# Kernel optimization log

Measured on AMD Instinct MI355X. Metric: run time of the kernel, lower is better.

## Reference

```python
import jax, jax.numpy as jnp
import numpy as np

N_HEAD = 12


def setup_inputs() -> dict:
    key = jax.random.key(0)
    ks = jax.random.split(key, 16)
    B, N, D, P, H = 1, 512, 384, 128, N_HEAD
    s = 0.02
    return {
        'x1d': jax.random.normal(ks[0], (B, N, D), jnp.float32),
        'x2d': jax.random.normal(ks[1], (B, N, N, P), jnp.float32),
        'pose_t': jax.random.normal(ks[2], (B, N, 3), jnp.float32),
        'pose_r': jax.random.normal(ks[3], (B, N, 3, 3), jnp.float32),
        'bias': jnp.zeros((B, 1, N, N), jnp.float32),
        'w_sq': jax.random.normal(ks[4], (D, D), jnp.float32) * s,
        'w_sk': jax.random.normal(ks[5], (D, D), jnp.float32) * s,
        'w_sv': jax.random.normal(ks[6], (D, D), jnp.float32) * s,
        'w_pb': jax.random.normal(ks[7], (P, H), jnp.float32) * s,
        'w_pq': jax.random.normal(ks[8], (D, H * 3 * 4), jnp.float32) * s,
        'w_pk': jax.random.normal(ks[9], (D, H * 3 * 4), jnp.float32) * s,
        'w_pv': jax.random.normal(ks[10], (D, H * 3 * 8), jnp.float32) * s,
        'tpw': jax.random.uniform(ks[11], (H,), jnp.float32),
        'w_pairv': jax.random.normal(ks[12], (P, D), jnp.float32) * s,
        'w_out': jax.random.normal(ks[13], (2 * D + H * 8 * 4, D), jnp.float32) * s,
        'b_out': jnp.zeros((D,), jnp.float32),
    }


def reference(x1d, x2d, pose_t, pose_r, bias, w_sq, w_sk, w_sv, w_pb,
              w_pq, w_pk, w_pv, tpw, w_pairv, w_out, b_out):
    B, N, D = x1d.shape
    H = N_HEAD
    dk = D // H
    scalar_w = 1.0 / np.sqrt(3 * dk)
    point_w_c = 1.0 / np.sqrt(3 * 4 * 9 / 2)
    pair_w = 1.0 / np.sqrt(3)

    T = pose_t                                # [B,N,3]
    R = jnp.swapaxes(pose_r, -1, -2)          # [B,N,3,3] (pose[1]^T as in torch code)

    # scalar attention
    q_s = (x1d @ w_sq).reshape(B, N, H, dk)
    k_s = (x1d @ w_sk).reshape(B, N, H, dk)
    v_s = (x1d @ w_sv).reshape(B, N, H, dk)
    scalar_attn = jnp.einsum('bihc,bjhc->bhij', q_s * scalar_w, k_s)

    # point attention (global frame)
    def affine(pt):  # R @ pt + T
        return jnp.einsum('bnxy,bnhpy->bnhpx', R, pt) + T[:, :, None, None, :]

    q_p = affine((x1d @ w_pq).reshape(B, N, H, 4, 3))
    k_p = affine((x1d @ w_pk).reshape(B, N, H, 4, 3))
    v_p = affine((x1d @ w_pv).reshape(B, N, H, 8, 3))

    dist = jnp.linalg.norm(q_p[:, :, None] - k_p[:, None], axis=-1)  # [B,I,J,H,P]
    pw = point_w_c * jax.nn.softplus(tpw)                            # [H]
    point_attn = -0.5 * pw[:, None, None] * jnp.transpose(dist.sum(-1), (0, 3, 1, 2))

    # pair bias attention
    pair_attn = pair_w * jnp.transpose(x2d @ w_pb, (0, 3, 1, 2))     # [B,H,I,J]

    attn = jax.nn.softmax(scalar_attn + point_attn + pair_attn + bias, axis=-1)

    # aggregations
    out_scalar = jnp.einsum('bhij,bjhc->bihc', attn, v_s).reshape(B, N, D)

    out_pg = jnp.einsum('bhij,bjhcp->bihcp', attn, v_p)              # [B,I,H,8,3]
    # inverse affine: R^T @ (x - T)
    out_pl = jnp.einsum('bnyx,bnhpy->bnhpx', R, out_pg - T[:, :, None, None, :])
    out_pn = jnp.linalg.norm(out_pl, axis=-1).reshape(B, N, H * 8)
    out_pl = out_pl.reshape(B, N, H * 8 * 3)

    v_pair = (x2d @ w_pairv).reshape(B, N, N, H, dk)
    out_pair = jnp.einsum('bhij,bijhc->bihc', attn, v_pair).reshape(B, N, D)

    feat = jnp.concatenate([out_scalar, out_pl, out_pair, out_pn], axis=-1)
    return feat @ w_out + b_out
```

## Files before the change

### kernel.cpp

```cpp
#include <hip/hip_runtime.h>
#include <hip/hip_bf16.h>
#include <math.h>

#define N_  512
#define D_  384
#define H_  12
#define DK_ 32
#define P_  128

typedef short short8 __attribute__((ext_vector_type(8)));
typedef float f32x4  __attribute__((ext_vector_type(4)));

static __device__ __forceinline__ unsigned short f2bf(float f) {
    union { float f; unsigned int u; } v; v.f = f;
    unsigned int r = (v.u + 0x7FFFu + ((v.u >> 16) & 1u)) >> 16;
    return (unsigned short)r;
}
static __device__ __forceinline__ float bf2f(unsigned short u) {
    union { unsigned int u; float f; } v; v.u = ((unsigned int)u) << 16;
    return v.f;
}
static __device__ __forceinline__ short2 pk2bf(float a, float b) {
    __hip_bfloat162 h = __float22bfloat162_rn(make_float2(a, b));
    return *(short2*)&h;
}
typedef union { short8 v; short2 h2[4]; } s8u;

__global__ __launch_bounds__(384) void k_front(
    const float* __restrict__ x2d, const float* __restrict__ w_pb,
    float* __restrict__ pairlog,
    const float* __restrict__ x1d, const float* __restrict__ pose_t,
    const float* __restrict__ pose_r,
    const float* __restrict__ w_sq, const float* __restrict__ w_sk,
    const float* __restrict__ w_sv, const float* __restrict__ w_pq,
    const float* __restrict__ w_pk, const float* __restrict__ w_pv,
    float* __restrict__ qs, float* __restrict__ kst,
    float* __restrict__ qp, float* __restrict__ kpt,
    unsigned short* __restrict__ vcatT)
{
    __shared__ float raw[8][288];
    __shared__ float Rsh[8][9];
    __shared__ float Tsh[8][3];

    const int t = threadIdx.x;

    if (blockIdx.x < 2048) {
        if (t >= 256) return;
        const int wid  = t >> 6;
        const int lane = t & 63;
        const int quad = lane >> 4;
        const int col  = lane & 15;
        const float pair_w = 0.57735027f;

        short8 bfr[4];
        #pragma unroll
        for (int kt = 0; kt < 4; ++kt) {
            #pragma unroll
            for (int jj = 0; jj < 8; ++jj) {
                int p = kt * 32 + quad * 8 + jj;
                bfr[kt][jj] = (col < 12) ? (short)f2bf(w_pb[p * 12 + col]) : (short)0;
            }
        }
        #pragma unroll
        for (int s = 0; s < 2; ++s) {
            const int T  = blockIdx.x * 8 + wid * 2 + s;
            const int i  = T >> 5;
            const int j0 = (T & 31) << 4;
            const float* xrow = x2d + ((size_t)(i * N_) + j0 + col) * P_;

            f32x4 acc = {0.f, 0.f, 0.f, 0.f};
            #pragma unroll
            for (int kt = 0; kt < 4; ++kt) {
                const int k0 = kt * 32 + quad * 8;
                float4 f0 = *(const float4*)(xrow + k0);
                float4 f1 = *(const float4*)(xrow + k0 + 4);
                s8u afr;
                afr.h2[0] = pk2bf(f0.x, f0.y);
                afr.h2[1] = pk2bf(f0.z, f0.w);
                afr.h2[2] = pk2bf(f1.x, f1.y);
                afr.h2[3] = pk2bf(f1.z, f1.w);
                acc = __builtin_amdgcn_mfma_f32_16x16x32_bf16(afr.v, bfr[kt], acc, 0, 0, 0);
            }
            if (col < 12) {
                #pragma unroll
                for (int r = 0; r < 4; ++r) {
                    int j = j0 + quad * 4 + r;
                    pairlog[((size_t)(col * N_ + i)) * N_ + j] = pair_w * acc[r];
                }
            }
        }
        return;
    }

    const int b   = blockIdx.x - 2048;
    const int seg = b >> 6;
    const int i0  = (b & 63) * 8;

    if (seg < 3) {
        const float* __restrict__ w = (seg == 0) ? w_sq : (seg == 1) ? w_sk : w_sv;
        float acc[8];
        #pragma unroll
        for (int r = 0; r < 8; ++r) acc[r] = 0.f;
        for (int d = 0; d < D_; d += 4) {
            float4 xr[8];
            #pragma unroll
            for (int r = 0; r < 8; ++r)
                xr[r] = *(const float4*)(x1d + (i0 + r) * D_ + d);
            #pragma unroll
            for (int e = 0; e < 4; ++e) {
                float wv = w[(d + e) * D_ + t];
                #pragma unroll
                for (int r = 0; r < 8; ++r)
                    acc[r] += ((const float*)&xr[r])[e] * wv;
            }
        }
        if (seg == 0) {
            #pragma unroll
            for (int r = 0; r < 8; ++r) qs[(i0 + r) * D_ + t] = acc[r];
        } else if (seg == 1) {
            *(float4*)(kst + t * N_ + i0)     = make_float4(acc[0], acc[1], acc[2], acc[3]);
            *(float4*)(kst + t * N_ + i0 + 4) = make_float4(acc[4], acc[5], acc[6], acc[7]);
        } else {
            int h = t >> 5, c = t & 31;
            s8u sv;
            #pragma unroll
            for (int r = 0; r < 4; ++r) sv.h2[r] = pk2bf(acc[2*r], acc[2*r+1]);
            *(short8*)(vcatT + ((size_t)h * 64 + c) * N_ + i0) = sv.v;
        }
    } else {
        if (t < 72) Rsh[t / 9][t % 9] = pose_r[(i0 + t / 9) * 9 + t % 9];
        else if (t < 96) {
            int r = (t - 72) / 3, c = (t - 72) % 3;
            Tsh[r][c] = pose_t[(i0 + r) * 3 + c];
        }

        if (t < 288) {
            const float* __restrict__ w;
            int col, ldw;
            if (seg == 3) {
                if (t < 144) { w = w_pq; col = t;       ldw = 144; }
                else         { w = w_pk; col = t - 144; ldw = 144; }
            } else         { w = w_pv; col = t;       ldw = 288; }
            float acc[8];
            #pragma unroll
            for (int r = 0; r < 8; ++r) acc[r] = 0.f;
            for (int d = 0; d < D_; d += 4) {
                float4 xr[8];
                #pragma unroll
                for (int r = 0; r < 8; ++r)
                    xr[r] = *(const float4*)(x1d + (i0 + r) * D_ + d);
                #pragma unroll
                for (int e = 0; e < 4; ++e) {
                    float wv = w[(d + e) * ldw + col];
                    #pragma unroll
                    for (int r = 0; r < 8; ++r)
                        acc[r] += ((const float*)&xr[r])[e] * wv;
                }
            }
            #pragma unroll
            for (int r = 0; r < 8; ++r) raw[r][t] = acc[r];
        }
        __syncthreads();

        if (t < 288) {
            const int x3   = t % 3;
            const int base = t - x3;
            if (seg == 3) {
                const int c = (t < 144) ? t : t - 144;
                if (t < 144) {
                    #pragma unroll
                    for (int r = 0; r < 8; ++r) {
                        float g = Rsh[r][0 + x3] * raw[r][base]
                                + Rsh[r][3 + x3] * raw[r][base + 1]
                                + Rsh[r][6 + x3] * raw[r][base + 2] + Tsh[r][x3];
                        qp[(i0 + r) * 144 + c] = g;
                    }
                } else {
                    float g[8];
                    #pragma unroll
                    for (int r = 0; r < 8; ++r)
                        g[r] = Rsh[r][0 + x3] * raw[r][base]
                             + Rsh[r][3 + x3] * raw[r][base + 1]
                             + Rsh[r][6 + x3] * raw[r][base + 2] + Tsh[r][x3];
                    *(float4*)(kpt + c * N_ + i0)     = make_float4(g[0], g[1], g[2], g[3]);
                    *(float4*)(kpt + c * N_ + i0 + 4) = make_float4(g[4], g[5], g[6], g[7]);
                }
            } else {
                int h = t / 24, pc = t % 24;
                float g[8];
                #pragma unroll
                for (int r = 0; r < 8; ++r)
                    g[r] = Rsh[r][0 + x3] * raw[r][base]
                         + Rsh[r][3 + x3] * raw[r][base + 1]
                         + Rsh[r][6 + x3] * raw[r][base + 2] + Tsh[r][x3];
                s8u sv;
                #pragma unroll
                for (int r = 0; r < 4; ++r) sv.h2[r] = pk2bf(g[2*r], g[2*r+1]);
                *(short8*)(vcatT + ((size_t)h * 64 + 32 + pc) * N_ + i0) = sv.v;
            }
        }
    }
}

__global__ __launch_bounds__(256) void k_sp_soft(
    const float* __restrict__ qs, const float* __restrict__ kst,
    const float* __restrict__ qp, const float* __restrict__ kpt,
    const float* __restrict__ bias, const float* __restrict__ tpw,
    const float* __restrict__ pairlog,
    unsigned short* __restrict__ attn_bf)
{
    const int h  = blockIdx.x / 128;
    const int i0 = (blockIdx.x % 128) * 4;
    const int t  = threadIdx.x;
    const int lane = t & 63;
    const int wid  = t >> 6;
    __shared__ float qsh[4][32];
    __shared__ float qph[4][12];
    __shared__ float wredm[4][4];
    __shared__ float wreds[4][4];
    if (t < 128) { int il = t / 32, c = t % 32; qsh[il][c] = qs[(i0+il) * D_ + h*32 + c]; }
    else if (t < 176) { int r = t - 128; int il = r / 12, c = r % 12; qph[il][c] = qp[(i0+il)*144 + h*12 + c]; }
    const float pwh = 0.13608276f * log1pf(expf(tpw[h]));
    const float scalar_w = 0.10206207f;
    __syncthreads();

    float v[4][2];
    for (int jh = 0; jh < 2; ++jh) {
        int j = t + jh * 256;
        float kv[32];
        #pragma unroll
        for (int c = 0; c < 32; ++c) kv[c] = kst[(h*32 + c) * N_ + j];
        float kp[12];
        #pragma unroll
        for (int c = 0; c < 12; ++c) kp[c] = kpt[(h*12 + c) * N_ + j];

        #pragma unroll
        for (int il = 0; il < 4; ++il) {
            float s = 0.f;
            #pragma unroll
            for (int c = 0; c < 32; ++c) s += qsh[il][c] * kv[c];
            float dsum = 0.f;
            #pragma unroll
            for (int p = 0; p < 4; ++p) {
                float dx = qph[il][p*3+0] - kp[p*3+0];
                float dy = qph[il][p*3+1] - kp[p*3+1];
                float dz = qph[il][p*3+2] - kp[p*3+2];
                dsum += sqrtf(dx*dx + dy*dy + dz*dz);
            }
            v[il][jh] = scalar_w * s - 0.5f * pwh * dsum
                      + bias[(i0+il) * N_ + j]
                      + pairlog[((size_t)(h * N_ + (i0+il))) * N_ + j];
        }
    }

    #pragma unroll
    for (int il = 0; il < 4; ++il) {
        float mt = fmaxf(v[il][0], v[il][1]);
        #pragma unroll
        for (int off = 1; off < 64; off <<= 1)
            mt = fmaxf(mt, __shfl_xor(mt, off));
        if (lane == 0) wredm[il][wid] = mt;
    }
    __syncthreads();
    float m[4];
    #pragma unroll
    for (int il = 0; il < 4; ++il)
        m[il] = fmaxf(fmaxf(wredm[il][0], wredm[il][1]),
                      fmaxf(wredm[il][2], wredm[il][3]));

    #pragma unroll
    for (int il = 0; il < 4; ++il) {
        float e0 = __expf(v[il][0] - m[il]);
        float e1 = __expf(v[il][1] - m[il]);
        v[il][0] = e0; v[il][1] = e1;
        float st = e0 + e1;
        #pragma unroll
        for (int off = 1; off < 64; off <<= 1)
            st += __shfl_xor(st, off);
        if (lane == 0) wreds[il][wid] = st;
    }
    __syncthreads();
    #pragma unroll
    for (int il = 0; il < 4; ++il) {
        float inv = 1.0f / (wreds[il][0] + wreds[il][1] + wreds[il][2] + wreds[il][3]);
        size_t base = ((size_t)(h * N_ + i0 + il)) * N_;
        attn_bf[base + t]       = f2bf(v[il][0] * inv);
        attn_bf[base + t + 256] = f2bf(v[il][1] * inv);
    }
}

__global__ __launch_bounds__(256) void k_mid(
    const unsigned short* __restrict__ attn_bf,
    const float* __restrict__ x2d,
    const unsigned short* __restrict__ vcatT,
    float* __restrict__ tmp,
    float* __restrict__ feat, float* __restrict__ outpg)
{
    __shared__ float4 at[3][N_];
    __shared__ float red[4][1536];

    const int t = threadIdx.x;

    if (blockIdx.x < 512) {
        const int i = blockIdx.x;
        for (int idx = t; idx < 12 * N_; idx += 256) {
            int h = idx >> 9, j = idx & 511;
            float a = bf2f(attn_bf[((size_t)(h * N_ + i)) * N_ + j]);
            ((float*)&at[h >> 2][j])[h & 3] = a;
        }
        __syncthreads();

        const int p2 = (t & 63) * 2;
        const int jh = t >> 6;
        float acc[12][2];
        #pragma unroll
        for (int h = 0; h < 12; ++h) { acc[h][0] = 0.f; acc[h][1] = 0.f; }
        const float* xb = x2d + (size_t)i * N_ * P_;

        #pragma unroll 4
        for (int j = jh; j < N_; j += 4) {
            float2 x = *(const float2*)(xb + j * P_ + p2);
            float4 a0 = at[0][j], a1 = at[1][j], a2 = at[2][j];
            acc[0][0]  += a0.x*x.x; acc[0][1]  += a0.x*x.y;
            acc[1][0]  += a0.y*x.x; acc[1][1]  += a0.y*x.y;
            acc[2][0]  += a0.z*x.x; acc[2][1]  += a0.z*x.y;
            acc[3][0]  += a0.w*x.x; acc[3][1]  += a0.w*x.y;
            acc[4][0]  += a1.x*x.x; acc[4][1]  += a1.x*x.y;
            acc[5][0]  += a1.y*x.x; acc[5][1]  += a1.y*x.y;
            acc[6][0]  += a1.z*x.x; acc[6][1]  += a1.z*x.y;
            acc[7][0]  += a1.w*x.x; acc[7][1]  += a1.w*x.y;
            acc[8][0]  += a2.x*x.x; acc[8][1]  += a2.x*x.y;
            acc[9][0]  += a2.y*x.x; acc[9][1]  += a2.y*x.y;
            acc[10][0] += a2.z*x.x; acc[10][1] += a2.z*x.y;
            acc[11][0] += a2.w*x.x; acc[11][1] += a2.w*x.y;
        }
        #pragma unroll
        for (int h = 0; h < 12; ++h) {
            red[jh][h * 128 + p2]     = acc[h][0];
            red[jh][h * 128 + p2 + 1] = acc[h][1];
        }
        __syncthreads();
        for (int idx = t; idx < 1536; idx += 256)
            tmp[(size_t)i * 1536 + idx] = red[0][idx] + red[1][idx] + red[2][idx] + red[3][idx];
        return;
    }

    const int bid  = blockIdx.x - 512;
    const int h    = bid >> 5;
    const int i0   = (bid & 31) << 4;
    const int wid  = t >> 6;
    const int lane = t & 63;
    const int quad = lane >> 4;
    const int col  = lane & 15;
    const int c    = wid * 16 + col;
    const bool cvalid = (c < 56);

    const unsigned short* arow = attn_bf + ((size_t)(h * N_ + i0 + col)) * N_;
    const unsigned short* brow = vcatT + ((size_t)h * 64 + c) * N_;

    f32x4 acc = {0.f, 0.f, 0.f, 0.f};
    #pragma unroll
    for (int kt = 0; kt < 16; ++kt) {
        const int k0 = kt * 32 + quad * 8;
        short8 a = *(const short8*)(arow + k0);
        short8 b;
        if (cvalid) b = *(const short8*)(brow + k0);
        else { b[0]=0;b[1]=0;b[2]=0;b[3]=0;b[4]=0;b[5]=0;b[6]=0;b[7]=0; }
        acc = __builtin_amdgcn_mfma_f32_16x16x32_bf16(a, b, acc, 0, 0, 0);
    }
    #pragma unroll
    for (int r = 0; r < 4; ++r) {
        int i = i0 + quad * 4 + r;
        if (c < 32)       feat[(size_t)i * 1152 + h * 32 + c] = acc[r];
        else if (c < 56)  outpg[((size_t)i * 12 + h) * 24 + (c - 32)] = acc[r];
    }
}

__global__ __launch_bounds__(384) void k_feat(
    const float* __restrict__ tmp, const float* __restrict__ outpg,
    const float* __restrict__ pose_t, const float* __restrict__ pose_r,
    const float* __restrict__ w_pairv, float* __restrict__ feat)
{
    const int i = blockIdx.x;
    const int t = threadIdx.x;
    __shared__ float tsh[1536];
    __shared__ float pg[288];
    __shared__ float pl[288];
    __shared__ float Rsh[9], Tsh[3];

    for (int idx = t; idx < 1536; idx += 384) tsh[idx] = tmp[(size_t)i * 1536 + idx];
    if (t < 288) pg[t] = outpg[i * 288 + t];
    if (t < 9) Rsh[t] = pose_r[i * 9 + t];
    if (t < 3) Tsh[t] = pose_t[i * 3 + t];
    __syncthreads();

    {
        int h = t >> 5;
        const float* ts = tsh + h * 128;
        float acc = 0.f;
        #pragma unroll 4
        for (int p = 0; p < 128; ++p) acc += ts[p] * w_pairv[p * D_ + t];
        feat[(size_t)i * 1152 + 672 + t] = acc;
    }
    if (t < 288) {
        int x3 = t % 3, base = t - x3;
        float g0 = pg[base + 0] - Tsh[0];
        float g1 = pg[base + 1] - Tsh[1];
        float g2 = pg[base + 2] - Tsh[2];
        float v = Rsh[x3*3+0]*g0 + Rsh[x3*3+1]*g1 + Rsh[x3*3+2]*g2;
        pl[t] = v;
        feat[(size_t)i * 1152 + 384 + t] = v;
    }
    __syncthreads();
    if (t < 96) {
        float a = pl[t*3], b = pl[t*3+1], c = pl[t*3+2];
        feat[(size_t)i * 1152 + 1056 + t] = sqrtf(a*a + b*b + c*c);
    }
}

__global__ __launch_bounds__(384) void k_out_part(
    const float* __restrict__ feat, const float* __restrict__ w_out,
    float* __restrict__ part)
{
    const int kc = blockIdx.x >> 6;
    const int i0 = (blockIdx.x & 63) * 8;
    const int t  = threadIdx.x;
    const int k0 = kc * 144;

    float acc[8];
    #pragma unroll
    for (int r = 0; r < 8; ++r) acc[r] = 0.f;

    for (int d = 0; d < 144; d += 4) {
        float4 fr[8];
        #pragma unroll
        for (int r = 0; r < 8; ++r)
            fr[r] = *(const float4*)(feat + (size_t)(i0 + r) * 1152 + k0 + d);
        #pragma unroll
        for (int e = 0; e < 4; ++e) {
            float wv = w_out[(size_t)(k0 + d + e) * D_ + t];
            #pragma unroll
            for (int r = 0; r < 8; ++r)
                acc[r] += ((const float*)&fr[r])[e] * wv;
        }
    }
    #pragma unroll
    for (int r = 0; r < 8; ++r)
        part[((size_t)kc * N_ + i0 + r) * D_ + t] = acc[r];
}

__global__ __launch_bounds__(256) void k_out_red(
    const float* __restrict__ part, const float* __restrict__ b_out,
    float* __restrict__ out)
{
    const int idx = blockIdx.x * 256 + threadIdx.x;
    float s = b_out[idx % D_];
    #pragma unroll
    for (int kc = 0; kc < 8; ++kc) s += part[(size_t)kc * (N_ * D_) + idx];
    out[idx] = s;
}

extern "C" void kernel_launch(void* const* d_in, const int* in_sizes, int n_in,
                              void* d_out, int out_size, void* d_ws, size_t ws_size,
                              hipStream_t stream)
{
    (void)in_sizes; (void)n_in; (void)out_size; (void)ws_size;
    const float* x1d     = (const float*)d_in[0];
    const float* x2d     = (const float*)d_in[1];
    const float* pose_t  = (const float*)d_in[2];
    const float* pose_r  = (const float*)d_in[3];
    const float* bias    = (const float*)d_in[4];
    const float* w_sq    = (const float*)d_in[5];
    const float* w_sk    = (const float*)d_in[6];
    const float* w_sv    = (const float*)d_in[7];
    const float* w_pb    = (const float*)d_in[8];
    const float* w_pq    = (const float*)d_in[9];
    const float* w_pk    = (const float*)d_in[10];
    const float* w_pv    = (const float*)d_in[11];
    const float* tpw     = (const float*)d_in[12];
    const float* w_pairv = (const float*)d_in[13];
    const float* w_out   = (const float*)d_in[14];
    const float* b_out   = (const float*)d_in[15];
    float* out = (float*)d_out;

    float* ws = (float*)d_ws;
    float* qs      = ws;
    float* kst     = qs      + 196608;
    float* qp      = kst     + 196608;
    float* kpt     = qp      + 73728;
    float* pairlog = kpt     + 73728;
    float* tmp     = pairlog + 3145728;
    float* outpg   = tmp     + 786432;
    float* feat    = outpg   + 147456;
    float* part    = feat    + 589824;
    unsigned short* attn_bf = (unsigned short*)(part + 1572864);
    unsigned short* vcatT   = attn_bf + (size_t)12 * N_ * N_;

    hipLaunchKernelGGL(k_front, dim3(2048 + 320), dim3(384), 0, stream,
                       x2d, w_pb, pairlog,
                       x1d, pose_t, pose_r, w_sq, w_sk, w_sv, w_pq, w_pk, w_pv,
                       qs, kst, qp, kpt, vcatT);
    hipLaunchKernelGGL(k_sp_soft, dim3(12 * 128), dim3(256), 0, stream,
                       qs, kst, qp, kpt, bias, tpw, pairlog, attn_bf);
    hipLaunchKernelGGL(k_mid, dim3(512 + 384), dim3(256), 0, stream,
                       attn_bf, x2d, vcatT, tmp, feat, outpg);
    hipLaunchKernelGGL(k_feat, dim3(N_), dim3(384), 0, stream,
                       tmp, outpg, pose_t, pose_r, w_pairv, feat);
    hipLaunchKernelGGL(k_out_part, dim3(512), dim3(384), 0, stream,
                       feat, w_out, part);
    hipLaunchKernelGGL(k_out_red, dim3(768), dim3(256), 0, stream,
                       part, b_out, out);
}
```

Measured before the change: 358.9 us.

## Split fused front kernel into pair and projection kernels; batch x2d loads

Splits the merged front kernel into two launches. k_pair uses 256 threads with a launch bound targeting four blocks per SM, so the old 384-thread blocks no longer carry 128 idle threads. k_pair also issues all x2d loads before the MFMA work, and the k_mid pair aggregation loop batches eight float2 loads per iteration, both to keep more memory requests in flight on these bandwidth-bound x2d streams. The cost is one extra kernel launch, the two front workloads no longer running concurrently, and higher register pressure.

```diff
diff --git a/kernel.cpp b/kernel.cpp
--- a/kernel.cpp
+++ b/kernel.cpp
@@ -26,9 +26,67 @@
 }
 typedef union { short8 v; short2 h2[4]; } s8u;
 
-__global__ __launch_bounds__(384) void k_front(
+__global__ __launch_bounds__(256, 4) void k_pair(
     const float* __restrict__ x2d, const float* __restrict__ w_pb,
-    float* __restrict__ pairlog,
+    float* __restrict__ pairlog)
+{
+    const int t    = threadIdx.x;
+    const int wid  = t >> 6;
+    const int lane = t & 63;
+    const int quad = lane >> 4;
+    const int col  = lane & 15;
+    const float pair_w = 0.57735027f;
+
+    short8 bfr[4];
+    #pragma unroll
+    for (int kt = 0; kt < 4; ++kt) {
+        #pragma unroll
+        for (int jj = 0; jj < 8; ++jj) {
+            int p = kt * 32 + quad * 8 + jj;
+            bfr[kt][jj] = (col < 12) ? (short)f2bf(w_pb[p * 12 + col]) : (short)0;
+        }
+    }
+
+    float4 xv[2][8];
+    #pragma unroll
+    for (int s = 0; s < 2; ++s) {
+        const int T  = blockIdx.x * 8 + wid * 2 + s;
+        const float* xrow = x2d + ((size_t)((T >> 5) * N_) + ((T & 31) << 4) + col) * P_;
+        #pragma unroll
+        for (int kt = 0; kt < 4; ++kt) {
+            xv[s][kt * 2 + 0] = *(const float4*)(xrow + kt * 32 + quad * 8);
+            xv[s][kt * 2 + 1] = *(const float4*)(xrow + kt * 32 + quad * 8 + 4);
+        }
+    }
+
+    #pragma unroll
+    for (int s = 0; s < 2; ++s) {
+        const int T  = blockIdx.x * 8 + wid * 2 + s;
+        const int i  = T >> 5;
+        const int j0 = (T & 31) << 4;
+        f32x4 acc = {0.f, 0.f, 0.f, 0.f};
+        #pragma unroll
+        for (int kt = 0; kt < 4; ++kt) {
+            float4 f0 = xv[s][kt * 2 + 0];
+            float4 f1 = xv[s][kt * 2 + 1];
+            s8u afr;
+            afr.h2[0] = pk2bf(f0.x, f0.y);
+            afr.h2[1] = pk2bf(f0.z, f0.w);
+            afr.h2[2] = pk2bf(f1.x, f1.y);
+            afr.h2[3] = pk2bf(f1.z, f1.w);
+            acc = __builtin_amdgcn_mfma_f32_16x16x32_bf16(afr.v, bfr[kt], acc, 0, 0, 0);
+        }
+        if (col < 12) {
+            #pragma unroll
+            for (int r = 0; r < 4; ++r) {
+                int j = j0 + quad * 4 + r;
+                pairlog[((size_t)(col * N_ + i)) * N_ + j] = pair_w * acc[r];
+            }
+        }
+    }
+}
+
+__global__ __launch_bounds__(384) void k_proj(
     const float* __restrict__ x1d, const float* __restrict__ pose_t,
     const float* __restrict__ pose_r,
     const float* __restrict__ w_sq, const float* __restrict__ w_sk,
@@ -38,63 +96,13 @@
     float* __restrict__ qp, float* __restrict__ kpt,
     unsigned short* __restrict__ vcatT)
 {
+    const int seg = blockIdx.y;
+    const int i0  = blockIdx.x * 8;
+    const int t   = threadIdx.x;
+
     __shared__ float raw[8][288];
     __shared__ float Rsh[8][9];
     __shared__ float Tsh[8][3];
-
-    const int t = threadIdx.x;
-
-    if (blockIdx.x < 2048) {
-        if (t >= 256) return;
-        const int wid  = t >> 6;
-        const int lane = t & 63;
-        const int quad = lane >> 4;
-        const int col  = lane & 15;
-        const float pair_w = 0.57735027f;
-
-        short8 bfr[4];
-        #pragma unroll
-        for (int kt = 0; kt < 4; ++kt) {
-            #pragma unroll
-            for (int jj = 0; jj < 8; ++jj) {
-                int p = kt * 32 + quad * 8 + jj;
-                bfr[kt][jj] = (col < 12) ? (short)f2bf(w_pb[p * 12 + col]) : (short)0;
-            }
-        }
-        #pragma unroll
-        for (int s = 0; s < 2; ++s) {
-            const int T  = blockIdx.x * 8 + wid * 2 + s;
-            const int i  = T >> 5;
-            const int j0 = (T & 31) << 4;
-            const float* xrow = x2d + ((size_t)(i * N_) + j0 + col) * P_;
-
-            f32x4 acc = {0.f, 0.f, 0.f, 0.f};
-            #pragma unroll
-            for (int kt = 0; kt < 4; ++kt) {
-                const int k0 = kt * 32 + quad * 8;
-                float4 f0 = *(const float4*)(xrow + k0);
-                float4 f1 = *(const float4*)(xrow + k0 + 4);
-                s8u afr;
-                afr.h2[0] = pk2bf(f0.x, f0.y);
-                afr.h2[1] = pk2bf(f0.z, f0.w);
-                afr.h2[2] = pk2bf(f1.x, f1.y);
-                afr.h2[3] = pk2bf(f1.z, f1.w);
-                acc = __builtin_amdgcn_mfma_f32_16x16x32_bf16(afr.v, bfr[kt], acc, 0, 0, 0);
-            }
-            if (col < 12) {
-                #pragma unroll
-                for (int r = 0; r < 4; ++r) {
-                    int j = j0 + quad * 4 + r;
-                    pairlog[((size_t)(col * N_ + i)) * N_ + j] = pair_w * acc[r];
-                }
-            }
-        }
-        return;
-    }
-
-    const int b   = blockIdx.x - 2048;
-    const int seg = b >> 6;
-    const int i0  = (b & 63) * 8;
 
     if (seg < 3) {
         const float* __restrict__ w = (seg == 0) ? w_sq : (seg == 1) ? w_sk : w_sv;
@@ -315,24 +323,31 @@
         float acc[12][2];
         #pragma unroll
         for (int h = 0; h < 12; ++h) { acc[h][0] = 0.f; acc[h][1] = 0.f; }
-        const float* xb = x2d + (size_t)i * N_ * P_;
-
-        #pragma unroll 4
-        for (int j = jh; j < N_; j += 4) {
-            float2 x = *(const float2*)(xb + j * P_ + p2);
-            float4 a0 = at[0][j], a1 = at[1][j], a2 = at[2][j];
-            acc[0][0]  += a0.x*x.x; acc[0][1]  += a0.x*x.y;
-            acc[1][0]  += a0.y*x.x; acc[1][1]  += a0.y*x.y;
-            acc[2][0]  += a0.z*x.x; acc[2][1]  += a0.z*x.y;
-            acc[3][0]  += a0.w*x.x; acc[3][1]  += a0.w*x.y;
-            acc[4][0]  += a1.x*x.x; acc[4][1]  += a1.x*x.y;
-            acc[5][0]  += a1.y*x.x; acc[5][1]  += a1.y*x.y;
-            acc[6][0]  += a1.z*x.x; acc[6][1]  += a1.z*x.y;
-            acc[7][0]  += a1.w*x.x; acc[7][1]  += a1.w*x.y;
-            acc[8][0]  += a2.x*x.x; acc[8][1]  += a2.x*x.y;
-            acc[9][0]  += a2.y*x.x; acc[9][1]  += a2.y*x.y;
-            acc[10][0] += a2.z*x.x; acc[10][1] += a2.z*x.y;
-            acc[11][0] += a2.w*x.x; acc[11][1] += a2.w*x.y;
+        const float* xb = x2d + (size_t)i * N_ * P_ + p2;
+
+        for (int j = jh; j < N_; j += 32) {
+            float2 x[8];
+            #pragma unroll
+            for (int u = 0; u < 8; ++u)
+                x[u] = *(const float2*)(xb + (j + u * 4) * P_);
+            #pragma unroll
+            for (int u = 0; u < 8; ++u) {
+                int jj = j + u * 4;
+                float4 a0 = at[0][jj], a1 = at[1][jj], a2 = at[2][jj];
+                float xx = x[u].x, xy = x[u].y;
+                acc[0][0]  += a0.x*xx; acc[0][1]  += a0.x*xy;
+                acc[1][0]  += a0.y*xx; acc[1][1]  += a0.y*xy;
+                acc[2][0]  += a0.z*xx; acc[2][1]  += a0.z*xy;
+                acc[3][0]  += a0.w*xx; acc[3][1]  += a0.w*xy;
+                acc[4][0]  += a1.x*xx; acc[4][1]  += a1.x*xy;
+                acc[5][0]  += a1.y*xx; acc[5][1]  += a1.y*xy;
+                acc[6][0]  += a1.z*xx; acc[6][1]  += a1.z*xy;
+                acc[7][0]  += a1.w*xx; acc[7][1]  += a1.w*xy;
+                acc[8][0]  += a2.x*xx; acc[8][1]  += a2.x*xy;
+                acc[9][0]  += a2.y*xx; acc[9][1]  += a2.y*xy;
+                acc[10][0] += a2.z*xx; acc[10][1] += a2.z*xy;
+                acc[11][0] += a2.w*xx; acc[11][1] += a2.w*xy;
+            }
         }
         #pragma unroll
         for (int h = 0; h < 12; ++h) {
@@ -496,8 +511,9 @@
     unsigned short* attn_bf = (unsigned short*)(part + 1572864);
     unsigned short* vcatT   = attn_bf + (size_t)12 * N_ * N_;
 
-    hipLaunchKernelGGL(k_front, dim3(2048 + 320), dim3(384), 0, stream,
-                       x2d, w_pb, pairlog,
+    hipLaunchKernelGGL(k_pair, dim3(2048), dim3(256), 0, stream,
+                       x2d, w_pb, pairlog);
+    hipLaunchKernelGGL(k_proj, dim3(64, 5), dim3(384), 0, stream,
                        x1d, pose_t, pose_r, w_sq, w_sk, w_sv, w_pq, w_pk, w_pv,
                        qs, kst, qp, kpt, vcatT);
     hipLaunchKernelGGL(k_sp_soft, dim3(12 * 128), dim3(256), 0, stream,
```

Result: slower. 381.2 us (+6.2%).
